# Kernel tuning notes

Measured on AMD Instinct MI355X. Metric: run time of the kernel, lower is better.

## Reference

```python
import jax, jax.numpy as jnp
import numpy as np

D_MODEL = 768
MLP_DIM = 3072
N_EXPERTS = 8
TOP_K = 2
GROUP_DET = 1024
GROUP_CLS = 128


def _route(x, wr, k, capacity):
    """Deterministic top-k softmax router with capacity (vmoe-style).

    x: [G, S, d], wr: [d, E]. Returns dispatch [G,S,E,C] (0/1) and
    combine [G,S,E,C] (gate-weighted).
    """
    G, S, _ = x.shape
    E = wr.shape[1]
    gates = jax.nn.softmax(jnp.einsum('gsd,de->gse', x, wr))  # [G,S,E]
    gval, gidx = jax.lax.top_k(gates, k)                      # [G,S,k]
    # rank-major ordering: all rank-0 choices first, then rank-1, ...
    idx = jnp.swapaxes(gidx, 1, 2).reshape(G, k * S)          # [G,kS]
    val = jnp.swapaxes(gval, 1, 2).reshape(G, k * S)
    oh = jax.nn.one_hot(idx, E, dtype=x.dtype)                # [G,kS,E]
    # position of each assignment in its expert's buffer
    pos = jnp.take_along_axis(jnp.cumsum(oh, axis=1), idx[..., None], axis=2)[..., 0] - 1.0
    keep = (pos < capacity).astype(x.dtype)                   # drop overflow tokens
    posc = jnp.where(pos < capacity, pos, 0.0).astype(jnp.int32)
    slot = jax.nn.one_hot(posc, capacity, dtype=x.dtype)      # [G,kS,C]
    disp = oh[:, :, :, None] * slot[:, :, None, :] * keep[:, :, None, None]  # [G,kS,E,C]
    disp = disp.reshape(G, k, S, E, capacity)
    combine = (disp * val.reshape(G, k, S, 1, 1)).sum(axis=1)  # [G,S,E,C]
    dispatch = disp.sum(axis=1)                                # [G,S,E,C]
    return dispatch, combine


def _expert_mlp(xe, w1, b1, w2, b2):
    # xe: [E,G,C,d]; per-expert params w1:[E,d,m], b1:[E,m], w2:[E,m,d], b2:[E,d]
    h = jax.nn.gelu(jnp.einsum('egcd,edm->egcm', xe, w1) + b1[:, None, None, :])
    return jnp.einsum('egcm,emd->egcd', h, w2) + b2[:, None, None, :]


def _moe_stream(x3, group_size, wr, w1, b1, w2, b2):
    B, S, d = x3.shape
    x = x3.reshape(-1, group_size, d)                         # [G,gs,d]
    capacity = group_size * TOP_K // N_EXPERTS
    dispatch, combine = _route(x, wr, TOP_K, capacity)
    xe = jnp.einsum('gsec,gsd->egcd', dispatch, x)            # gather to experts
    ye = _expert_mlp(xe, w1, b1, w2, b2)                      # grouped MLP
    y = jnp.einsum('gsec,egcd->gsd', combine, ye)             # weighted scatter back
    return y.reshape(B, S, d)


def setup_inputs() -> dict:
    key = jax.random.key(0)
    ks = jax.random.split(key, 8)
    xav1 = float(np.sqrt(6.0 / (D_MODEL + MLP_DIM)))
    xavr = float(np.sqrt(6.0 / (D_MODEL + N_EXPERTS)))
    return {
        'inputs_det': jax.random.normal(ks[0], (8, 1024, D_MODEL), jnp.float32),
        'inputs_cls': jax.random.normal(ks[1], (8, 128, D_MODEL), jnp.float32),
        'wr_det': jax.random.uniform(ks[2], (D_MODEL, N_EXPERTS), jnp.float32, -xavr, xavr),
        'wr_cls': jax.random.uniform(ks[3], (D_MODEL, N_EXPERTS), jnp.float32, -xavr, xavr),
        'w1': jax.random.uniform(ks[4], (N_EXPERTS, D_MODEL, MLP_DIM), jnp.float32, -xav1, xav1),
        'b1': jax.random.normal(ks[5], (N_EXPERTS, MLP_DIM), jnp.float32) * 1e-6,
        'w2': jax.random.uniform(ks[6], (N_EXPERTS, MLP_DIM, D_MODEL), jnp.float32, -xav1, xav1),
        'b2': jax.random.normal(ks[7], (N_EXPERTS, D_MODEL), jnp.float32) * 1e-6,
    }


def reference(inputs_det, inputs_cls, wr_det, wr_cls, w1, b1, w2, b2):
    out_det = _moe_stream(inputs_det, GROUP_DET, wr_det, w1, b1, w2, b2)
    out_cls = _moe_stream(inputs_cls, GROUP_CLS, wr_cls, w1, b1, w2, b2)
    return (out_det, out_cls)
```

## Files before the change

kernel.cpp:

```cpp
#include <hip/hip_runtime.h>
#include <hip/hip_bf16.h>
#include <math.h>

typedef __bf16 bf16;
typedef __bf16 bf16x8 __attribute__((ext_vector_type(8)));
typedef __bf16 bf16x4 __attribute__((ext_vector_type(4)));
typedef float  f32x4  __attribute__((ext_vector_type(4)));

#define D_MODEL 768
#define MLP_DIM 3072

#define SZ_W1T   ((size_t)8*3072*768*2)
#define SZ_W2T   ((size_t)8*768*3072*2)
#define SZ_XED   ((size_t)8*8*256*768*2)
#define SZ_XEC   ((size_t)8*8*32*768*2)
#define SZ_HD    ((size_t)8*2048*3072*2)
#define SZ_HC    ((size_t)8*256*3072*2)
#define SZ_YED   ((size_t)8*2048*768*2)
#define SZ_YEC   ((size_t)8*256*768*2)
#define SZ_RID   ((size_t)8192*8)
#define SZ_RGD   ((size_t)8192*8)
#define SZ_RIC   ((size_t)1024*8)
#define SZ_RGC   ((size_t)1024*8)
#define SZ_STD   ((size_t)8*8*256*4)
#define SZ_STC   ((size_t)8*8*32*4)
#define SZ_TSD   ((size_t)2*8192*4)
#define SZ_TSC   ((size_t)2*1024*4)

#define OFF_W1T  ((size_t)0)
#define OFF_W2T  (OFF_W1T + SZ_W1T)
#define OFF_XED  (OFF_W2T + SZ_W2T)
#define OFF_XEC  (OFF_XED + SZ_XED)
#define OFF_HD   (OFF_XEC + SZ_XEC)
#define OFF_HC   (OFF_HD  + SZ_HD)
#define OFF_YED  (OFF_HC  + SZ_HC)
#define OFF_YEC  (OFF_YED + SZ_YED)
#define OFF_RID  (OFF_YEC + SZ_YEC)
#define OFF_RGD  (OFF_RID + SZ_RID)
#define OFF_RIC  (OFF_RGD + SZ_RGD)
#define OFF_RGC  (OFF_RIC + SZ_RIC)
#define OFF_STD  (OFF_RGC + SZ_RGC)
#define OFF_STC  (OFF_STD + SZ_STD)
#define OFF_TSD  (OFF_STC + SZ_STC)
#define OFF_TSC  (OFF_TSD + SZ_TSD)

__device__ __forceinline__ void lds_load16(const void* g, void* l) {
  __builtin_amdgcn_global_load_lds((__attribute__((address_space(1))) void*)g,
                                   (__attribute__((address_space(3))) void*)l,
                                   16, 0, 0);
}

__device__ __forceinline__ float gelu_fast(float x) {
  float y = 0.7978845608028654f * x * (1.f + 0.044715f * x * x);
  float e = __expf(2.f * y);
  float t = 1.f - 2.f / (e + 1.f);
  return 0.5f * x * (1.f + t);
}

__global__ void router_kernel(const float* __restrict__ xd, const float* __restrict__ wrd,
                              const float* __restrict__ xc, const float* __restrict__ wrc,
                              int2* __restrict__ rid, float2* __restrict__ rgd,
                              int2* __restrict__ ric, float2* __restrict__ rgc,
                              int splitd) {
  int bid = blockIdx.x;
  const float *x, *wr; int2* ridx; float2* rgate;
  if (bid < splitd) { x = xd; wr = wrd; ridx = rid; rgate = rgd; }
  else { bid -= splitd; x = xc; wr = wrc; ridx = ric; rgate = rgc; }
  int wave = threadIdx.x >> 6;
  int lane = threadIdx.x & 63;
  int t = bid * 4 + wave;
  const float* xr = x + (size_t)t * D_MODEL;
  float acc[8];
#pragma unroll
  for (int e = 0; e < 8; ++e) acc[e] = 0.f;
  for (int d = lane; d < D_MODEL; d += 64) {
    float xv = xr[d];
    const float* w = wr + d * 8;
    float4 a = *(const float4*)w;
    float4 b = *(const float4*)(w + 4);
    acc[0] += xv * a.x; acc[1] += xv * a.y; acc[2] += xv * a.z; acc[3] += xv * a.w;
    acc[4] += xv * b.x; acc[5] += xv * b.y; acc[6] += xv * b.z; acc[7] += xv * b.w;
  }
#pragma unroll
  for (int off = 32; off > 0; off >>= 1) {
#pragma unroll
    for (int e = 0; e < 8; ++e) acc[e] += __shfl_xor(acc[e], off, 64);
  }
  float mx = acc[0];
#pragma unroll
  for (int e = 1; e < 8; ++e) mx = fmaxf(mx, acc[e]);
  float p[8]; float z = 0.f;
#pragma unroll
  for (int e = 0; e < 8; ++e) { p[e] = __expf(acc[e] - mx); z += p[e]; }
  int i1 = 0;
#pragma unroll
  for (int e = 1; e < 8; ++e) if (p[e] > p[i1]) i1 = e;
  int i2 = (i1 == 0) ? 1 : 0;
#pragma unroll
  for (int e = 0; e < 8; ++e) if (e != i1 && p[e] > p[i2]) i2 = e;
  if (lane == 0) {
    float inv = 1.f / z;
    ridx[t]  = make_int2(i1, i2);
    rgate[t] = make_float2(p[i1] * inv, p[i2] * inv);
  }
}

__global__ void positions_kernel(const int2* __restrict__ rid, int* __restrict__ std_,
                                 int* __restrict__ tsd_, const int2* __restrict__ ric,
                                 int* __restrict__ stc_, int* __restrict__ tsc_) {
  __shared__ int2 sh[1024];
  int bid = blockIdx.x;
  const int2* ridx; int *slot_token, *tok_slot; int S, C, g;
  if (bid < 8) { ridx = rid; slot_token = std_; tok_slot = tsd_; S = 1024; C = 256; g = bid; }
  else { ridx = ric; slot_token = stc_; tok_slot = tsc_; S = 128; C = 32; g = bid - 8; }
  int lane = threadIdx.x;
  int ntok = 8 * S;
  for (int i = lane; i < S; i += 64) sh[i] = ridx[g * S + i];
  __builtin_amdgcn_s_waitcnt(0);
  unsigned long long ltmask = (1ull << lane) - 1ull;
  int cnt[8];
#pragma unroll
  for (int e = 0; e < 8; ++e) cnt[e] = 0;
  int nch = (2 * S) >> 6;
  for (int ch = 0; ch < nch; ++ch) {
    int a = (ch << 6) + lane;
    int r = (a >= S) ? 1 : 0;
    int s = a - r * S;
    int2 id = sh[s];
    int  e  = r ? id.y : id.x;
    unsigned long long mymask = 0;
    int add[8];
#pragma unroll
    for (int ee = 0; ee < 8; ++ee) {
      unsigned long long mk = __ballot(e == ee);
      if (e == ee) mymask = mk;
      add[ee] = __popcll(mk);
    }
    int pos = cnt[e] + __popcll(mymask & ltmask);
    int sl = (e * 8 + g) * C + pos;
    if (pos < C) slot_token[sl] = s;
    tok_slot[r * ntok + g * S + s] = (pos < C) ? sl : -1;
#pragma unroll
    for (int ee = 0; ee < 8; ++ee) cnt[ee] += add[ee];
  }
}

__global__ void gather_kernel(const float* __restrict__ xd, const int* __restrict__ std_,
                              bf16* __restrict__ xed, const float* __restrict__ xc,
                              const int* __restrict__ stc_, bf16* __restrict__ xec,
                              int splitd) {
  int bid = blockIdx.x;
  const float* x; const int* slot_token; bf16* xe; int S, C;
  if (bid < splitd) { x = xd; slot_token = std_; xe = xed; S = 1024; C = 256; }
  else { bid -= splitd; x = xc; slot_token = stc_; xe = xec; S = 128; C = 32; }
  int slot = bid * 4 + (threadIdx.x >> 6);
  int lane = threadIdx.x & 63;
  int g = (slot / C) & 7;
  int s = slot_token[slot];
  bf16* dst = xe + (size_t)slot * D_MODEL;
  const float* xr = x + ((size_t)g * S + (s < 0 ? 0 : s)) * D_MODEL;
#pragma unroll
  for (int j = 0; j < 3; ++j) {
    int idx = j * 256 + lane * 4;
    float4 v;
    if (s >= 0) v = *(const float4*)(xr + idx);
    else        v = make_float4(0.f, 0.f, 0.f, 0.f);
    bf16 o[4] = {(bf16)v.x, (bf16)v.y, (bf16)v.z, (bf16)v.w};
    *(uint2*)(dst + idx) = *(const uint2*)o;
  }
}

__global__ void convt_kernel(const float* __restrict__ w1, bf16* __restrict__ w1t,
                             const float* __restrict__ w2, bf16* __restrict__ w2t) {
  __shared__ float tile[32][33];
  int bid = blockIdx.x;
  const float* src; bf16* dst; int K, N;
  if (bid < 18432) { src = w1; dst = w1t; K = 768; N = 3072; }
  else { bid -= 18432; src = w2; dst = w2t; K = 3072; N = 768; }
  int e = bid / 2304;
  int t = bid - e * 2304;
  int tiles_x = N >> 5;
  int ky = t / tiles_x;
  int n0 = (t - ky * tiles_x) * 32, k0 = ky * 32;
  const float* S_ = src + (size_t)e * K * N;
  bf16* D_ = dst + (size_t)e * K * N;
  int tx = threadIdx.x & 31, ty = threadIdx.x >> 5;
#pragma unroll
  for (int i = 0; i < 4; ++i)
    tile[ty + 8 * i][tx] = S_[(size_t)(k0 + ty + 8 * i) * N + (n0 + tx)];
  __syncthreads();
  int tid = threadIdx.x;
  int n = tid >> 3, kc = (tid & 7) * 4;
  bf16 o[4] = {(bf16)tile[kc][n], (bf16)tile[kc + 1][n], (bf16)tile[kc + 2][n], (bf16)tile[kc + 3][n]};
  *(uint2*)(D_ + (size_t)(n0 + n) * K + (k0 + kc)) = *(const uint2*)o;
}

__global__ void combine_kernel(const int* __restrict__ tsd_, const float2* __restrict__ rgd,
                               const bf16* __restrict__ yed, float* __restrict__ outd,
                               const int* __restrict__ tsc_, const float2* __restrict__ rgc,
                               const bf16* __restrict__ yec, float* __restrict__ outc,
                               int splitd) {
  int bid = blockIdx.x;
  const int* tok_slot; const float2* rgate; const bf16* ye; float* out; int ntok;
  if (bid < splitd) { tok_slot = tsd_; rgate = rgd; ye = yed; out = outd; ntok = 8192; }
  else { bid -= splitd; tok_slot = tsc_; rgate = rgc; ye = yec; out = outc; ntok = 1024; }
  int t = bid * 4 + (threadIdx.x >> 6);
  int lane = threadIdx.x & 63;
  int s1 = tok_slot[t];
  int s2 = tok_slot[ntok + t];
  float2 gg = rgate[t];
  float g1 = (s1 < 0) ? 0.f : gg.x;
  float g2 = (s2 < 0) ? 0.f : gg.y;
  const bf16* y1 = ye + (size_t)(s1 < 0 ? 0 : s1) * D_MODEL;
  const bf16* y2 = ye + (size_t)(s2 < 0 ? 0 : s2) * D_MODEL;
  float* orow = out + (size_t)t * D_MODEL;
#pragma unroll
  for (int j = 0; j < 3; ++j) {
    int idx = j * 256 + lane * 4;
    bf16x4 a = *(const bf16x4*)(y1 + idx);
    bf16x4 b = *(const bf16x4*)(y2 + idx);
    float4 o;
    o.x = g1 * (float)a[0] + g2 * (float)b[0];
    o.y = g1 * (float)a[1] + g2 * (float)b[1];
    o.z = g1 * (float)a[2] + g2 * (float)b[2];
    o.w = g1 * (float)a[3] + g2 * (float)b[3];
    *(float4*)(orow + idx) = o;
  }
}

template <int GELU>
__launch_bounds__(256, 3)
__global__ void gemm_mfma(const bf16* __restrict__ Adet, const bf16* __restrict__ Acls,
                          const bf16* __restrict__ Btall, const float* __restrict__ biasall,
                          int Mdet, int Mcls, int N, int K,
                          int Nmd, int Nmc, int Nn, int minner, int splitd,
                          bf16* __restrict__ Odet, bf16* __restrict__ Ocls) {
  int bid = blockIdx.x;
  const bf16* Aall; bf16* Oall; int M, Nm;
  if (bid < splitd) { Aall = Adet; Oall = Odet; M = Mdet; Nm = Nmd; }
  else { bid -= splitd; Aall = Acls; Oall = Ocls; M = Mcls; Nm = Nmc; }
  const int e   = bid & 7;
  const int seq = bid >> 3;
  int m_t, n_t;
  if (minner) { n_t = seq / Nm; m_t = seq - n_t * Nm; }
  else        { m_t = seq / Nn; n_t = seq - m_t * Nn; }
  const int n0 = n_t * 128;
  const int m0 = m_t * 128;
  const int tid  = threadIdx.x;
  const int wave = tid >> 6, lane = tid & 63;
  const int wm = (wave >> 1) * 64, wn = (wave & 1) * 64;
  const int lrow = lane & 15, lquad = lane >> 4;

  __shared__ __align__(16) bf16 smem[16384];
  bf16* As = smem;
  bf16* Bs = smem + 8192;

  const bf16* A  = Aall  + (size_t)e * M * K;
  const bf16* Bt = Btall + (size_t)e * N * K;

  const int srow = tid >> 3;
  const int gq   = (tid & 7) ^ (srow & 7);
  const bf16* Asrc = A  + (size_t)(m0 + srow) * K + gq * 8;
  const bf16* Bsrc = Bt + (size_t)(n0 + srow) * K + gq * 8;
  char* AsB = (char*)As;
  char* BsB = (char*)Bs;
  const int ldsw = wave * 1024;

  const float* bias = biasall + (size_t)e * N;
  float bfr[4];
#pragma unroll
  for (int ni = 0; ni < 4; ++ni) bfr[ni] = bias[n0 + wn + ni * 16 + lrow];

  f32x4 acc[4][4];
#pragma unroll
  for (int mi = 0; mi < 4; ++mi)
#pragma unroll
    for (int ni = 0; ni < 4; ++ni) acc[mi][ni] = {0.f, 0.f, 0.f, 0.f};

  const int xsw = lrow & 7;
  const int nsteps = K >> 6;
  for (int kt = 0; kt < nsteps; ++kt) {
    const bf16* a0 = Asrc + kt * 64;
    const bf16* b0 = Bsrc + kt * 64;
#pragma unroll
    for (int rd = 0; rd < 4; ++rd) {
      lds_load16(a0 + (size_t)(rd * 32) * K, AsB + rd * 4096 + ldsw);
      lds_load16(b0 + (size_t)(rd * 32) * K, BsB + rd * 4096 + ldsw);
    }
    __syncthreads();
#pragma unroll
    for (int h = 0; h < 2; ++h) {
      bf16x8 fa[4], fb[4];
      const int ca = ((h * 4 + lquad) ^ xsw) * 8;
#pragma unroll
      for (int i = 0; i < 4; ++i) {
        fa[i] = *(const bf16x8*)(As + (wm + i * 16 + lrow) * 64 + ca);
        fb[i] = *(const bf16x8*)(Bs + (wn + i * 16 + lrow) * 64 + ca);
      }
#pragma unroll
      for (int mi = 0; mi < 4; ++mi)
#pragma unroll
        for (int ni = 0; ni < 4; ++ni)
          acc[mi][ni] = __builtin_amdgcn_mfma_f32_16x16x32_bf16(fa[mi], fb[ni], acc[mi][ni], 0, 0, 0);
    }
    __syncthreads();
  }

#pragma unroll
  for (int mi = 0; mi < 4; ++mi) {
#pragma unroll
    for (int r = 0; r < 4; ++r) {
      int row = wm + mi * 16 + lquad * 4 + r;
#pragma unroll
      for (int ni = 0; ni < 4; ++ni) {
        int colL = wn + ni * 16 + lrow;
        float v = acc[mi][ni][r] + bfr[ni];
        if (GELU) v = gelu_fast(v);
        int chunk = (colL >> 3) ^ (row & 7);
        smem[row * 128 + chunk * 8 + (colL & 7)] = (bf16)v;
      }
    }
  }
  __syncthreads();
  bf16* O = Oall + (size_t)e * M * N;
#pragma unroll
  for (int it = 0; it < 8; ++it) {
    int idx = it * 256 + tid;
    int row = idx >> 4;
    int ck  = idx & 15;
    int pchunk = ck ^ (row & 7);
    bf16x8 vv = *(const bf16x8*)(smem + row * 128 + pchunk * 8);
    *(bf16x8*)(O + (size_t)(m0 + row) * N + n0 + ck * 8) = vv;
  }
}

extern "C" void kernel_launch(void* const* d_in, const int* in_sizes, int n_in,
                              void* d_out, int out_size, void* d_ws, size_t ws_size,
                              hipStream_t stream) {
  (void)in_sizes; (void)n_in; (void)ws_size; (void)out_size;
  const float* x_det  = (const float*)d_in[0];
  const float* x_cls  = (const float*)d_in[1];
  const float* wr_det = (const float*)d_in[2];
  const float* wr_cls = (const float*)d_in[3];
  const float* w1     = (const float*)d_in[4];
  const float* b1     = (const float*)d_in[5];
  const float* w2     = (const float*)d_in[6];
  const float* b2     = (const float*)d_in[7];
  float* out = (float*)d_out;
  char*  ws  = (char*)d_ws;

  bf16*   w1t    = (bf16*)(ws + OFF_W1T);
  bf16*   w2t    = (bf16*)(ws + OFF_W2T);
  bf16*   xe_det = (bf16*)(ws + OFF_XED);
  bf16*   xe_cls = (bf16*)(ws + OFF_XEC);
  bf16*   h_det  = (bf16*)(ws + OFF_HD);
  bf16*   h_cls  = (bf16*)(ws + OFF_HC);
  bf16*   ye_det = (bf16*)(ws + OFF_YED);
  bf16*   ye_cls = (bf16*)(ws + OFF_YEC);
  int2*   ri_det = (int2*)(ws + OFF_RID);
  float2* rg_det = (float2*)(ws + OFF_RGD);
  int2*   ri_cls = (int2*)(ws + OFF_RIC);
  float2* rg_cls = (float2*)(ws + OFF_RGC);
  int*    st_det = (int*)(ws + OFF_STD);
  int*    st_cls = (int*)(ws + OFF_STC);
  int*    ts_det = (int*)(ws + OFF_TSD);
  int*    ts_cls = (int*)(ws + OFF_TSC);

  hipMemsetAsync(ws + OFF_STD, 0xFF, SZ_STD + SZ_STC, stream);

  convt_kernel<<<2 * 18432, 256, 0, stream>>>(w1, w1t, w2, w2t);

  router_kernel<<<2048 + 256, 256, 0, stream>>>(x_det, wr_det, x_cls, wr_cls,
                                                ri_det, rg_det, ri_cls, rg_cls, 2048);
  positions_kernel<<<16, 64, 0, stream>>>(ri_det, st_det, ts_det, ri_cls, st_cls, ts_cls);

  gather_kernel<<<4096 + 512, 256, 0, stream>>>(x_det, st_det, xe_det, x_cls, st_cls, xe_cls, 4096);

  gemm_mfma<1><<<8 * 16 * 24 + 8 * 2 * 24, 256, 0, stream>>>(
      xe_det, xe_cls, w1t, b1, 2048, 256, 3072, 768,
      16, 2, 24, 1, 8 * 16 * 24, h_det, h_cls);

  gemm_mfma<0><<<8 * 16 * 6 + 8 * 2 * 6, 256, 0, stream>>>(
      h_det, h_cls, w2t, b2, 2048, 256, 768, 3072,
      16, 2, 6, 0, 8 * 16 * 6, ye_det, ye_cls);

  combine_kernel<<<2048 + 256, 256, 0, stream>>>(ts_det, rg_det, ye_det, out,
                                                 ts_cls, rg_cls, ye_cls,
                                                 out + (size_t)8192 * 768, 2048);
}
```

Measured before the change: 483.7 us.

## Enlarge expert GEMM tiles to 256x256 with double-buffered LDS ping-pong pipeline

Reworks the grouped expert GEMM to use 256x256 output tiles computed by 512-thread blocks of 8 waves. It stages two K-steps at a time into a double-buffered 128 KB LDS area with explicit vmcnt waits and barriers, so global-to-LDS copies overlap MFMA work, and it raises wave priority around the MFMA bursts. Larger tiles cut the global traffic per FLOP. In exchange, the block count drops sharply (the second GEMM gets only 216 blocks), LDS pressure limits each CU to about one block, and the hand-written synchronisation is fragile.

```diff
diff --git a/kernel.cpp b/kernel.cpp
--- a/kernel.cpp
+++ b/kernel.cpp
@@ -229,7 +229,7 @@
 }
 
 template <int GELU>
-__launch_bounds__(256, 3)
+__launch_bounds__(512, 2)
 __global__ void gemm_mfma(const bf16* __restrict__ Adet, const bf16* __restrict__ Acls,
                           const bf16* __restrict__ Btall, const float* __restrict__ biasall,
                           int Mdet, int Mcls, int N, int K,
@@ -244,70 +244,121 @@
   int m_t, n_t;
   if (minner) { n_t = seq / Nm; m_t = seq - n_t * Nm; }
   else        { m_t = seq / Nn; n_t = seq - m_t * Nn; }
-  const int n0 = n_t * 128;
-  const int m0 = m_t * 128;
+  const int n0 = n_t * 256;
+  const int m0 = m_t * 256;
   const int tid  = threadIdx.x;
   const int wave = tid >> 6, lane = tid & 63;
-  const int wm = (wave >> 1) * 64, wn = (wave & 1) * 64;
+  const int wm = (wave >> 2) * 128, wn = (wave & 3) * 64;
   const int lrow = lane & 15, lquad = lane >> 4;
 
-  __shared__ __align__(16) bf16 smem[16384];
-  bf16* As = smem;
-  bf16* Bs = smem + 8192;
+  __shared__ __align__(16) bf16 smem[65536];
+  char* smemB = (char*)smem;
 
   const bf16* A  = Aall  + (size_t)e * M * K;
   const bf16* Bt = Btall + (size_t)e * N * K;
 
-  const int srow = tid >> 3;
-  const int gq   = (tid & 7) ^ (srow & 7);
-  const bf16* Asrc = A  + (size_t)(m0 + srow) * K + gq * 8;
-  const bf16* Bsrc = Bt + (size_t)(n0 + srow) * K + gq * 8;
-  char* AsB = (char*)As;
-  char* BsB = (char*)Bs;
+  const int srow0 = tid >> 3;
+  const int gq    = (tid & 7) ^ (srow0 & 7);
+  const bf16* Asrc = A  + (size_t)(m0 + srow0) * K + gq * 8;
+  const bf16* Bsrc = Bt + (size_t)(n0 + srow0) * K + gq * 8;
   const int ldsw = wave * 1024;
+
+  const int aBase = (wm ? 8192 : 0) + lrow * 64;
+  const int bBase = 16384 + (wn >= 128 ? 8192 : 0) + (wn & 64) * 64 + lrow * 64;
+  const int ca0 = (lquad ^ (lrow & 7)) * 8;
+  const int ca1 = ca0 ^ 32;
 
   const float* bias = biasall + (size_t)e * N;
   float bfr[4];
 #pragma unroll
   for (int ni = 0; ni < 4; ++ni) bfr[ni] = bias[n0 + wn + ni * 16 + lrow];
 
-  f32x4 acc[4][4];
-#pragma unroll
-  for (int mi = 0; mi < 4; ++mi)
+  f32x4 acc[8][4];
+#pragma unroll
+  for (int mi = 0; mi < 8; ++mi)
 #pragma unroll
     for (int ni = 0; ni < 4; ++ni) acc[mi][ni] = {0.f, 0.f, 0.f, 0.f};
 
-  const int xsw = lrow & 7;
-  const int nsteps = K >> 6;
-  for (int kt = 0; kt < nsteps; ++kt) {
-    const bf16* a0 = Asrc + kt * 64;
-    const bf16* b0 = Bsrc + kt * 64;
-#pragma unroll
-    for (int rd = 0; rd < 4; ++rd) {
-      lds_load16(a0 + (size_t)(rd * 32) * K, AsB + rd * 4096 + ldsw);
-      lds_load16(b0 + (size_t)(rd * 32) * K, BsB + rd * 4096 + ldsw);
-    }
-    __syncthreads();
-#pragma unroll
-    for (int h = 0; h < 2; ++h) {
-      bf16x8 fa[4], fb[4];
-      const int ca = ((h * 4 + lquad) ^ xsw) * 8;
-#pragma unroll
-      for (int i = 0; i < 4; ++i) {
-        fa[i] = *(const bf16x8*)(As + (wm + i * 16 + lrow) * 64 + ca);
-        fb[i] = *(const bf16x8*)(Bs + (wn + i * 16 + lrow) * 64 + ca);
-      }
-#pragma unroll
-      for (int mi = 0; mi < 4; ++mi)
-#pragma unroll
-        for (int ni = 0; ni < 4; ++ni)
-          acc[mi][ni] = __builtin_amdgcn_mfma_f32_16x16x32_bf16(fa[mi], fb[ni], acc[mi][ni], 0, 0, 0);
-    }
-    __syncthreads();
-  }
-
-#pragma unroll
-  for (int mi = 0; mi < 4; ++mi) {
+  bf16x8 fa[2][4], fb0[2][2], fb1[2][2];
+
+#define STG_A(buf, half, kt) do { \
+    const bf16* _s = Asrc + (size_t)((half) * 128) * K + (size_t)(kt) * 64; \
+    char* _d = smemB + (buf) * 65536 + (half) * 16384 + ldsw; \
+    lds_load16(_s, _d); \
+    lds_load16(_s + (size_t)64 * K, _d + 8192); \
+  } while (0)
+#define STG_B(buf, half, kt) do { \
+    const bf16* _s = Bsrc + (size_t)((half) * 128) * K + (size_t)(kt) * 64; \
+    char* _d = smemB + (buf) * 65536 + 32768 + (half) * 16384 + ldsw; \
+    lds_load16(_s, _d); \
+    lds_load16(_s + (size_t)64 * K, _d + 8192); \
+  } while (0)
+#define LDA(buf, qm) do { \
+    const bf16* _p = smem + (buf) * 32768 + aBase + (qm) * 4096; \
+    _Pragma("unroll") \
+    for (int _i = 0; _i < 4; ++_i) { \
+      fa[0][_i] = *(const bf16x8*)(_p + _i * 1024 + ca0); \
+      fa[1][_i] = *(const bf16x8*)(_p + _i * 1024 + ca1); \
+    } \
+  } while (0)
+#define LDB(buf, qn, FB) do { \
+    const bf16* _p = smem + (buf) * 32768 + bBase + (qn) * 2048; \
+    _Pragma("unroll") \
+    for (int _j = 0; _j < 2; ++_j) { \
+      FB[0][_j] = *(const bf16x8*)(_p + _j * 1024 + ca0); \
+      FB[1][_j] = *(const bf16x8*)(_p + _j * 1024 + ca1); \
+    } \
+  } while (0)
+#define MM(qm, qn, FB) do { \
+    __builtin_amdgcn_s_setprio(1); \
+    _Pragma("unroll") \
+    for (int _h = 0; _h < 2; ++_h) \
+      _Pragma("unroll") \
+      for (int _i = 0; _i < 4; ++_i) \
+        _Pragma("unroll") \
+        for (int _j = 0; _j < 2; ++_j) \
+          acc[(qm) * 4 + _i][(qn) * 2 + _j] = __builtin_amdgcn_mfma_f32_16x16x32_bf16( \
+              fa[_h][_i], FB[_h][_j], acc[(qm) * 4 + _i][(qn) * 2 + _j], 0, 0, 0); \
+    __builtin_amdgcn_s_setprio(0); \
+  } while (0)
+#define BAR() __builtin_amdgcn_s_barrier()
+#define VMC4() asm volatile("s_waitcnt vmcnt(4)" ::: "memory")
+
+  const int nt = K >> 6;
+  const int niter = nt >> 1;
+
+  STG_B(0, 0, 0); STG_B(0, 1, 0); STG_A(0, 0, 0); STG_A(0, 1, 0);
+  STG_B(1, 0, 1); STG_B(1, 1, 1);
+  VMC4();
+  BAR();
+
+  for (int it = 0; it < niter; ++it) {
+    const int k1 = 2 * it + 1;
+    const int k2 = (2 * it + 2 < nt) ? 2 * it + 2 : nt - 1;
+    const int k3 = (2 * it + 3 < nt) ? 2 * it + 3 : nt - 1;
+    LDA(0, 0); LDB(0, 0, fb0); STG_A(1, 0, k1); BAR(); MM(0, 0, fb0); BAR();
+    LDB(0, 1, fb1);            STG_A(1, 1, k1); BAR(); MM(0, 1, fb1); BAR();
+    LDA(0, 1);                 STG_B(0, 0, k2); BAR(); MM(1, 1, fb1); BAR();
+                               STG_B(0, 1, k2); VMC4();
+                                                BAR(); MM(1, 0, fb0); BAR();
+    LDA(1, 0); LDB(1, 0, fb0); STG_A(0, 0, k2); BAR(); MM(0, 0, fb0); BAR();
+    LDB(1, 1, fb1);            STG_A(0, 1, k2); BAR(); MM(0, 1, fb1); BAR();
+    LDA(1, 1);                 STG_B(1, 0, k3); BAR(); MM(1, 1, fb1); BAR();
+                               STG_B(1, 1, k3); VMC4();
+                                                BAR(); MM(1, 0, fb0); BAR();
+  }
+
+#undef STG_A
+#undef STG_B
+#undef LDA
+#undef LDB
+#undef MM
+#undef BAR
+#undef VMC4
+
+  __syncthreads();
+#pragma unroll
+  for (int mi = 0; mi < 8; ++mi) {
 #pragma unroll
     for (int r = 0; r < 4; ++r) {
       int row = wm + mi * 16 + lquad * 4 + r;
@@ -317,19 +368,19 @@
         float v = acc[mi][ni][r] + bfr[ni];
         if (GELU) v = gelu_fast(v);
         int chunk = (colL >> 3) ^ (row & 7);
-        smem[row * 128 + chunk * 8 + (colL & 7)] = (bf16)v;
+        smem[row * 256 + chunk * 8 + (colL & 7)] = (bf16)v;
       }
     }
   }
   __syncthreads();
   bf16* O = Oall + (size_t)e * M * N;
 #pragma unroll
-  for (int it = 0; it < 8; ++it) {
-    int idx = it * 256 + tid;
-    int row = idx >> 4;
-    int ck  = idx & 15;
+  for (int itw = 0; itw < 16; ++itw) {
+    int idx = itw * 512 + tid;
+    int row = idx >> 5;
+    int ck  = idx & 31;
     int pchunk = ck ^ (row & 7);
-    bf16x8 vv = *(const bf16x8*)(smem + row * 128 + pchunk * 8);
+    bf16x8 vv = *(const bf16x8*)(smem + row * 256 + pchunk * 8);
     *(bf16x8*)(O + (size_t)(m0 + row) * N + n0 + ck * 8) = vv;
   }
 }
@@ -376,13 +427,13 @@
 
   gather_kernel<<<4096 + 512, 256, 0, stream>>>(x_det, st_det, xe_det, x_cls, st_cls, xe_cls, 4096);
 
-  gemm_mfma<1><<<8 * 16 * 24 + 8 * 2 * 24, 256, 0, stream>>>(
+  gemm_mfma<1><<<8 * 8 * 12 + 8 * 1 * 12, 512, 0, stream>>>(
       xe_det, xe_cls, w1t, b1, 2048, 256, 3072, 768,
-      16, 2, 24, 1, 8 * 16 * 24, h_det, h_cls);
-
-  gemm_mfma<0><<<8 * 16 * 6 + 8 * 2 * 6, 256, 0, stream>>>(
+      8, 1, 12, 1, 8 * 8 * 12, h_det, h_cls);
+
+  gemm_mfma<0><<<8 * 8 * 3 + 8 * 1 * 3, 512, 0, stream>>>(
       h_det, h_cls, w2t, b2, 2048, 256, 768, 3072,
-      16, 2, 6, 0, 8 * 16 * 6, ye_det, ye_cls);
+      8, 1, 3, 0, 8 * 8 * 3, ye_det, ye_cls);
 
   combine_kernel<<<2048 + 256, 256, 0, stream>>>(ts_det, rg_det, ye_det, out,
                                                  ts_cls, rg_cls, ye_cls,
```

Result: no change. 486.4 us (+0.6%).
